# Kernel optimization log

Hardware: AMD Instinct MI355X
Metric: run time of the kernel (lower is better)

Reference implementation:

```python
import jax, jax.numpy as jnp
import numpy as np

B, S, F_IN = 8, 2048, 1024
H, SC = 512, 256
N_LAYERS = 3


def _glorot(key, shape):
    fan_in, fan_out = shape[-2], shape[-1]
    lim = float(np.sqrt(6.0 / (fan_in + fan_out)))
    return jax.random.uniform(key, shape, jnp.float32, -lim, lim)


def setup_inputs() -> dict:
    key = jax.random.key(0)
    ks = jax.random.split(key, 8)
    x = jax.random.normal(ks[0], (B, S, F_IN), jnp.float32)
    Wp = _glorot(ks[1], (F_IN, H)); bp = jnp.zeros((H,), jnp.float32)
    gcn_W = _glorot(ks[2], (N_LAYERS, H, H)); gcn_b = jnp.zeros((N_LAYERS, H), jnp.float32)
    s1_W = _glorot(ks[3], (H, SC)); s1_b = jnp.zeros((SC,), jnp.float32)
    s2_W = _glorot(ks[4], (SC, SC // 2)); s2_b = jnp.zeros((SC // 2,), jnp.float32)
    s3_W = _glorot(ks[5], (SC // 2, 1)); s3_b = jnp.zeros((1,), jnp.float32)
    return {"x": x, "Wp": Wp, "bp": bp, "gcn_W": gcn_W, "gcn_b": gcn_b,
            "s1_W": s1_W, "s1_b": s1_b, "s2_W": s2_W, "s2_b": s2_b,
            "s3_W": s3_W, "s3_b": s3_b}


def _build_adj(seq_len):
    # tridiagonal band: self + immediate temporal neighbors
    a = jnp.eye(seq_len, dtype=jnp.float32)
    a = a + jnp.eye(seq_len, k=1, dtype=jnp.float32) + jnp.eye(seq_len, k=-1, dtype=jnp.float32)
    deg = a.sum(axis=1)
    dinv = jnp.power(deg + 1e-8, -0.5)
    # D^{-1/2} A D^{-1/2}
    return dinv[:, None] * a * dinv[None, :]


def reference(x, Wp, bp, gcn_W, gcn_b, s1_W, s1_b, s2_W, s2_b, s3_W, s3_b):
    seq_len = x.shape[1]
    adj = _build_adj(seq_len)  # [S, S]
    h = jnp.einsum('bsf,fh->bsh', x, Wp) + bp  # feature projection
    for i in range(N_LAYERS):
        support = jnp.einsum('bsh,hk->bsk', h, gcn_W[i])
        h = jnp.einsum('st,btk->bsk', adj, support) + gcn_b[i]
        if i < N_LAYERS - 1:
            h = jax.nn.relu(h)  # dropout is identity in eval mode
    z = jax.nn.relu(jnp.einsum('bsh,hc->bsc', h, s1_W) + s1_b)
    z = jax.nn.relu(jnp.einsum('bsc,cd->bsd', z, s2_W) + s2_b)
    scores = jax.nn.sigmoid(jnp.einsum('bsd,do->bso', z, s3_W) + s3_b)
    return scores[..., 0]  # [B, S]
```

## Files before the change

kernel.cpp:

```cpp
#include <hip/hip_runtime.h>
#include <hip/hip_fp16.h>
#include <cstdint>
#include <cstddef>


typedef _Float16 f16;
typedef _Float16 f16x8 __attribute__((ext_vector_type(8)));
typedef float    f32x4 __attribute__((ext_vector_type(4)));

__device__ __forceinline__ void async_cp16(const void* g, void* l) {
  __builtin_amdgcn_global_load_lds((const __attribute__((address_space(1))) void*)g,
                                   (__attribute__((address_space(3))) void*)l, 16, 0, 0);
}

__device__ __forceinline__ f16x8 splat8(f16 v) {
  f16x8 r;
#pragma unroll
  for (int e = 0; e < 8; ++e) r[e] = v;
  return r;
}

template<int BM, int BN, int WAVES_M, int WAVES_N, bool RELU, bool HAS_BIAS, int AMODE>
__global__ __launch_bounds__(256, 4) void gemm_f16_kernel(
    const void* __restrict__ Aptr, const f16* __restrict__ BT,
    f16* __restrict__ C, const float* __restrict__ bias,
    int M, int N, int K)
{
  constexpr int BK = 64;
  constexpr int WM = BM / WAVES_M;
  constexpr int WN = BN / WAVES_N;
  constexpr int TM = WM / 16;
  constexpr int TN = WN / 16;
  constexpr int ITER_A = (BM * BK) / (256 * 8);
  constexpr int ITER_B = (BN * BK) / (256 * 8);
  constexpr int S = 2048;

  __shared__ __align__(16) f16 sA[BM * BK];
  __shared__ __align__(16) f16 sB[BN * BK];

  const int tid  = threadIdx.x;
  const int lane = tid & 63;
  const int wave = tid >> 6;
  const int wm   = wave / WAVES_N;
  const int wn   = wave % WAVES_N;
  const int m0   = blockIdx.x * BM;
  const int n0   = blockIdx.y * BN;

  uint32_t offA[ITER_A][3];
  f16      cfA[ITER_A][3];
  const float dM = 0.57735026919f;
  const float dE = 0.70710678118f;
#pragma unroll
  for (int j = 0; j < ITER_A; ++j) {
    const int linear = j * 256 + tid;
    const int row = linear >> 3;
    const int q   = (linear & 7) ^ (row & 7);
    const int gm  = m0 + row;
    if constexpr (AMODE == 1) {
      offA[j][0] = (uint32_t)(((size_t)gm * K + q * 8) * 4);
    } else {
      const int s = gm & (S - 1);
      const float dsv = (s == 0 || s == S - 1) ? dE : dM;
      const float cpf = (s > 0)     ? dsv * ((s - 1 == 0) ? dE : dM)     : 0.0f;
      const float csf = dsv * dsv;
      const float cnf = (s < S - 1) ? dsv * ((s + 1 == S - 1) ? dE : dM) : 0.0f;
      const int rm1 = (s > 0)     ? gm - 1 : gm;
      const int rp1 = (s < S - 1) ? gm + 1 : gm;
      offA[j][0] = (uint32_t)(((size_t)rm1 * K + q * 8) * 2);
      offA[j][1] = (uint32_t)(((size_t)gm  * K + q * 8) * 2);
      offA[j][2] = (uint32_t)(((size_t)rp1 * K + q * 8) * 2);
      cfA[j][0] = (f16)cpf; cfA[j][1] = (f16)csf; cfA[j][2] = (f16)cnf;
    }
  }

  f32x4 acc[TM][TN];
#pragma unroll
  for (int i = 0; i < TM; ++i)
#pragma unroll
    for (int j = 0; j < TN; ++j)
      acc[i][j] = (f32x4){0.f, 0.f, 0.f, 0.f};

  const int quad = lane >> 4;
  const int l16  = lane & 15;

  for (int kt = 0; kt < K; kt += BK) {
    __syncthreads();
#pragma unroll
    for (int j = 0; j < ITER_B; ++j) {
      const int linear = j * 256 + tid;
      const int row = linear >> 3;
      const int q   = (linear & 7) ^ (row & 7);
      async_cp16(BT + (size_t)(n0 + row) * K + kt + q * 8, &sB[linear * 8]);
    }
    if constexpr (AMODE == 1) {
      const char* base = (const char*)Aptr + (size_t)kt * 4;
#pragma unroll
      for (int j = 0; j < ITER_A; ++j) {
        const float4* p = (const float4*)(base + offA[j][0]);
        const float4 a = p[0], b = p[1];
        f16x8 o;
        o[0] = (f16)a.x;  o[1] = (f16)a.y;  o[2] = (f16)a.z;  o[3] = (f16)a.w;
        o[4] = (f16)b.x;  o[5] = (f16)b.y;  o[6] = (f16)b.z;  o[7] = (f16)b.w;
        *(f16x8*)&sA[(size_t)(j * 256 + tid) * 8] = o;
      }
    } else {
      const char* base = (const char*)Aptr + (size_t)kt * 2;
#pragma unroll
      for (int j = 0; j < ITER_A; ++j) {
        f16x8 pv = *(const f16x8*)(base + offA[j][0]);
        f16x8 sv = *(const f16x8*)(base + offA[j][1]);
        f16x8 nv = *(const f16x8*)(base + offA[j][2]);
        f16x8 r = pv * splat8(cfA[j][0]);
        r += sv * splat8(cfA[j][1]);
        r += nv * splat8(cfA[j][2]);
        *(f16x8*)&sA[(size_t)(j * 256 + tid) * 8] = r;
      }
    }
    __syncthreads();

#pragma unroll
    for (int kk = 0; kk < 2; ++kk) {
      const int c = quad + kk * 4;
      f16x8 af[TM], bf[TN];
#pragma unroll
      for (int mi = 0; mi < TM; ++mi) {
        const int ml = wm * WM + mi * 16 + l16;
        af[mi] = *(const f16x8*)&sA[ml * 64 + ((c ^ (ml & 7)) * 8)];
      }
#pragma unroll
      for (int ni = 0; ni < TN; ++ni) {
        const int nl = wn * WN + ni * 16 + l16;
        bf[ni] = *(const f16x8*)&sB[nl * 64 + ((c ^ (nl & 7)) * 8)];
      }
#pragma unroll
      for (int mi = 0; mi < TM; ++mi)
#pragma unroll
        for (int ni = 0; ni < TN; ++ni)
          acc[mi][ni] = __builtin_amdgcn_mfma_f32_16x16x32_f16(
              af[mi], bf[ni], acc[mi][ni], 0, 0, 0);
    }
  }

#pragma unroll
  for (int ni = 0; ni < TN; ++ni) {
    const int nc = n0 + wn * WN + ni * 16 + l16;
    const float bv = HAS_BIAS ? bias[nc] : 0.0f;
#pragma unroll
    for (int mi = 0; mi < TM; ++mi) {
#pragma unroll
      for (int r = 0; r < 4; ++r) {
        const int mr = m0 + wm * WM + mi * 16 + quad * 4 + r;
        float v = acc[mi][ni][r] + bv;
        if (RELU) v = fmaxf(v, 0.0f);
        C[(size_t)mr * N + nc] = (f16)v;
      }
    }
  }
}

__global__ __launch_bounds__(256) void head_fused_kernel(
    const f16* __restrict__ h, const f16* __restrict__ S1T,
    const f16* __restrict__ S2T,
    const float* __restrict__ s1b, const float* __restrict__ s2b,
    const float* __restrict__ s3w, const float* __restrict__ s3b,
    float* __restrict__ out)
{
  __shared__ __align__(16) char smem[36864 + 32 * 264 * 2];
  f16* sA  = (f16*)smem;
  f16* sB  = (f16*)(smem + 4096);
  f16* zs  = (f16*)(smem + 36864);
  f16* z2s = (f16*)smem;
  f16* sB2 = (f16*)(smem + 8704);

  const int tid  = threadIdx.x;
  const int lane = tid & 63;
  const int wave = tid >> 6;
  const int quad = lane >> 4;
  const int l16  = lane & 15;
  const int m0   = blockIdx.x * 32;

  f32x4 acc[2][4];
#pragma unroll
  for (int i = 0; i < 2; ++i)
#pragma unroll
    for (int j = 0; j < 4; ++j) acc[i][j] = (f32x4){0.f, 0.f, 0.f, 0.f};

  for (int kt = 0; kt < 512; kt += 64) {
    __syncthreads();
    {
      const int linear = tid;
      const int row = linear >> 3;
      const int q   = (linear & 7) ^ (row & 7);
      async_cp16(h + (size_t)(m0 + row) * 512 + kt + q * 8, &sA[linear * 8]);
    }
#pragma unroll
    for (int j = 0; j < 8; ++j) {
      const int linear = j * 256 + tid;
      const int row = linear >> 3;
      const int q   = (linear & 7) ^ (row & 7);
      async_cp16(S1T + (size_t)row * 512 + kt + q * 8, &sB[linear * 8]);
    }
    __syncthreads();
#pragma unroll
    for (int kk = 0; kk < 2; ++kk) {
      const int c = quad + kk * 4;
      f16x8 af[2], bf[4];
#pragma unroll
      for (int mi = 0; mi < 2; ++mi) {
        const int ml = mi * 16 + l16;
        af[mi] = *(const f16x8*)&sA[ml * 64 + ((c ^ (ml & 7)) * 8)];
      }
#pragma unroll
      for (int ni = 0; ni < 4; ++ni) {
        const int nl = wave * 64 + ni * 16 + l16;
        bf[ni] = *(const f16x8*)&sB[nl * 64 + ((c ^ (nl & 7)) * 8)];
      }
#pragma unroll
      for (int mi = 0; mi < 2; ++mi)
#pragma unroll
        for (int ni = 0; ni < 4; ++ni)
          acc[mi][ni] = __builtin_amdgcn_mfma_f32_16x16x32_f16(
              af[mi], bf[ni], acc[mi][ni], 0, 0, 0);
    }
  }
#pragma unroll
  for (int ni = 0; ni < 4; ++ni) {
    const int nc = wave * 64 + ni * 16 + l16;
    const float bv = s1b[nc];
#pragma unroll
    for (int mi = 0; mi < 2; ++mi)
#pragma unroll
      for (int r = 0; r < 4; ++r) {
        const int row = mi * 16 + quad * 4 + r;
        zs[row * 264 + nc] = (f16)fmaxf(acc[mi][ni][r] + bv, 0.0f);
      }
  }
  __syncthreads();

  f32x4 acc2[2][2];
#pragma unroll
  for (int i = 0; i < 2; ++i)
#pragma unroll
    for (int j = 0; j < 2; ++j) acc2[i][j] = (f32x4){0.f, 0.f, 0.f, 0.f};

  for (int kt2 = 0; kt2 < 4; ++kt2) {
    __syncthreads();
#pragma unroll
    for (int j = 0; j < 4; ++j) {
      const int linear = j * 256 + tid;
      const int row = linear >> 3;
      const int q   = (linear & 7) ^ (row & 7);
      async_cp16(S2T + (size_t)row * 256 + kt2 * 64 + q * 8, &sB2[linear * 8]);
    }
    __syncthreads();
#pragma unroll
    for (int kk = 0; kk < 2; ++kk) {
      const int c = quad + kk * 4;
      f16x8 af[2], bf[2];
#pragma unroll
      for (int mi = 0; mi < 2; ++mi) {
        const int row = mi * 16 + l16;
        af[mi] = *(const f16x8*)&zs[row * 264 + (kt2 * 8 + c) * 8];
      }
#pragma unroll
      for (int ni = 0; ni < 2; ++ni) {
        const int nl = wave * 32 + ni * 16 + l16;
        bf[ni] = *(const f16x8*)&sB2[nl * 64 + ((c ^ (nl & 7)) * 8)];
      }
#pragma unroll
      for (int mi = 0; mi < 2; ++mi)
#pragma unroll
        for (int ni = 0; ni < 2; ++ni)
          acc2[mi][ni] = __builtin_amdgcn_mfma_f32_16x16x32_f16(
              af[mi], bf[ni], acc2[mi][ni], 0, 0, 0);
    }
  }
  __syncthreads();
#pragma unroll
  for (int ni = 0; ni < 2; ++ni) {
    const int nc = wave * 32 + ni * 16 + l16;
    const float bv = s2b[nc];
#pragma unroll
    for (int mi = 0; mi < 2; ++mi)
#pragma unroll
      for (int r = 0; r < 4; ++r) {
        const int row = mi * 16 + quad * 4 + r;
        z2s[row * 136 + nc] = (f16)fmaxf(acc2[mi][ni][r] + bv, 0.0f);
      }
  }
  __syncthreads();

  const int m  = tid >> 3;
  const int qd = tid & 7;
  float p = 0.f;
#pragma unroll
  for (int j = 0; j < 2; ++j) {
    f16x8 v = *(const f16x8*)&z2s[m * 136 + qd * 16 + j * 8];
#pragma unroll
    for (int e = 0; e < 8; ++e) p += (float)v[e] * s3w[qd * 16 + j * 8 + e];
  }
  p += __shfl_xor(p, 1);
  p += __shfl_xor(p, 2);
  p += __shfl_xor(p, 4);
  if (qd == 0) out[m0 + m] = 1.0f / (1.0f + expf(-(p + s3b[0])));
}

__global__ __launch_bounds__(256) void prep_kernel(
    const float* __restrict__ Wp, f16* __restrict__ WpT,
    const float* __restrict__ gW, f16* __restrict__ GT,
    const float* __restrict__ s1W, f16* __restrict__ S1T,
    const float* __restrict__ s2W, f16* __restrict__ S2T)
{
  __shared__ f16 s[64 * 68];
  const int tid = threadIdx.x;
  int b = blockIdx.x;

  const float* W; f16* WT; int K, N, tile;
  if (b < 128)      { W = Wp;  WT = WpT; K = 1024; N = 512; tile = b; }
  else if (b < 320) { const int i = (b - 128) >> 6;
                      W = gW + (size_t)i * 262144; WT = GT + (size_t)i * 262144;
                      K = 512; N = 512; tile = (b - 128) & 63; }
  else if (b < 352) { W = s1W; WT = S1T; K = 512; N = 256; tile = b - 320; }
  else              { W = s2W; WT = S2T; K = 256; N = 128; tile = b - 352; }

  const int nt = tile % (N >> 6);
  const int kt = tile / (N >> 6);
#pragma unroll
  for (int it = 0; it < 16; ++it) {
    const int i  = it * 256 + tid;
    const int rk = i >> 6, rn = i & 63;
    s[rn * 68 + rk] = (f16)W[(size_t)(kt * 64 + rk) * N + nt * 64 + rn];
  }
  __syncthreads();
#pragma unroll
  for (int it = 0; it < 16; ++it) {
    const int i  = it * 256 + tid;
    const int rn = i >> 6, rk = i & 63;
    WT[(size_t)(nt * 64 + rn) * K + kt * 64 + rk] = s[rn * 68 + rk];
  }
}

extern "C" void kernel_launch(void* const* d_in, const int* in_sizes, int n_in,
                              void* d_out, int out_size, void* d_ws, size_t ws_size,
                              hipStream_t stream) {
  (void)in_sizes; (void)n_in; (void)out_size; (void)ws_size;
  const float* x   = (const float*)d_in[0];
  const float* Wp  = (const float*)d_in[1];
  const float* bp  = (const float*)d_in[2];
  const float* gW  = (const float*)d_in[3];
  const float* gb  = (const float*)d_in[4];
  const float* s1W = (const float*)d_in[5];
  const float* s1b = (const float*)d_in[6];
  const float* s2W = (const float*)d_in[7];
  const float* s2b = (const float*)d_in[8];
  const float* s3W = (const float*)d_in[9];
  const float* s3b = (const float*)d_in[10];
  float* out = (float*)d_out;

  constexpr int M = 16384;
  char* ws = (char*)d_ws;
  f16* hA  = (f16*)(ws + 0);
  f16* hB  = (f16*)(ws + 16777216);
  f16* WpT = (f16*)(ws + 33554432);
  f16* GT  = (f16*)(ws + 34603008);
  f16* S1T = (f16*)(ws + 36175872);
  f16* S2T = (f16*)(ws + 36438016);

  prep_kernel<<<360, 256, 0, stream>>>(Wp, WpT, gW, GT, s1W, S1T, s2W, S2T);

  gemm_f16_kernel<32, 256, 1, 4, false, true, 1>
      <<<dim3(M / 32, 2), 256, 0, stream>>>(x, WpT, hA, bp, M, 512, 1024);

  gemm_f16_kernel<32, 256, 1, 4, true, true, 2>
      <<<dim3(M / 32, 2), 256, 0, stream>>>(hA, GT, hB, gb, M, 512, 512);
  gemm_f16_kernel<32, 256, 1, 4, true, true, 2>
      <<<dim3(M / 32, 2), 256, 0, stream>>>(hB, GT + 262144, hA, gb + 512, M, 512, 512);
  gemm_f16_kernel<32, 256, 1, 4, false, true, 2>
      <<<dim3(M / 32, 2), 256, 0, stream>>>(hA, GT + 524288, hB, gb + 1024, M, 512, 512);

  head_fused_kernel<<<M / 32, 256, 0, stream>>>(hB, S1T, S2T, s1b, s2b, s3W, s3b, out);
}
```

Before: 222.0 us.

## Enlarge GEMM tiles, load halo rows into LDS, register-prefetch fp32 input

Moves the GEMMs to 64x256 tiles with 512 threads in a 2x4 wave grid. For the GCN layers, the raw A rows plus a one-row halo are copied into LDS asynchronously, and the tridiagonal stencil is applied when fragments are read from LDS. Before, each thread did three global loads per chunk. For the projection GEMM, the next K-tile of fp32 x is prefetched into registers during the MFMA loop. The cost is more LDS reads and stencil math per fragment, repeated across the N-waves, plus higher register pressure with 512-thread blocks.

```diff
diff --git a/kernel.cpp b/kernel.cpp
--- a/kernel.cpp
+++ b/kernel.cpp
@@ -20,22 +20,24 @@
   return r;
 }
 
-template<int BM, int BN, int WAVES_M, int WAVES_N, bool RELU, bool HAS_BIAS, int AMODE>
-__global__ __launch_bounds__(256, 4) void gemm_f16_kernel(
+template<int BM, int BN, bool RELU, bool HAS_BIAS, int AMODE>
+__global__ __launch_bounds__(512, 4) void gemm_f16_kernel(
     const void* __restrict__ Aptr, const f16* __restrict__ BT,
     f16* __restrict__ C, const float* __restrict__ bias,
     int M, int N, int K)
 {
   constexpr int BK = 64;
+  constexpr int NT = 512;
+  constexpr int WAVES_M = 2, WAVES_N = 4;
   constexpr int WM = BM / WAVES_M;
   constexpr int WN = BN / WAVES_N;
   constexpr int TM = WM / 16;
   constexpr int TN = WN / 16;
-  constexpr int ITER_A = (BM * BK) / (256 * 8);
-  constexpr int ITER_B = (BN * BK) / (256 * 8);
+  constexpr int ITER_B = (BN * BK) / (NT * 8);
   constexpr int S = 2048;
-
-  __shared__ __align__(16) f16 sA[BM * BK];
+  constexpr int AROWS = (AMODE == 2) ? (BM + 2) : BM;
+
+  __shared__ __align__(16) f16 sA[AROWS * BK];
   __shared__ __align__(16) f16 sB[BN * BK];
 
   const int tid  = threadIdx.x;
@@ -45,32 +47,31 @@
   const int wn   = wave % WAVES_N;
   const int m0   = blockIdx.x * BM;
   const int n0   = blockIdx.y * BN;
-
-  uint32_t offA[ITER_A][3];
-  f16      cfA[ITER_A][3];
+  const int quad = lane >> 4;
+  const int l16  = lane & 15;
+
   const float dM = 0.57735026919f;
   const float dE = 0.70710678118f;
-#pragma unroll
-  for (int j = 0; j < ITER_A; ++j) {
-    const int linear = j * 256 + tid;
-    const int row = linear >> 3;
-    const int q   = (linear & 7) ^ (row & 7);
-    const int gm  = m0 + row;
-    if constexpr (AMODE == 1) {
-      offA[j][0] = (uint32_t)(((size_t)gm * K + q * 8) * 4);
-    } else {
-      const int s = gm & (S - 1);
+
+  f16 cf[TM][3];
+  if constexpr (AMODE == 2) {
+#pragma unroll
+    for (int mi = 0; mi < TM; ++mi) {
+      const int grow = m0 + wm * WM + mi * 16 + l16;
+      const int s = grow & (S - 1);
       const float dsv = (s == 0 || s == S - 1) ? dE : dM;
-      const float cpf = (s > 0)     ? dsv * ((s - 1 == 0) ? dE : dM)     : 0.0f;
-      const float csf = dsv * dsv;
-      const float cnf = (s < S - 1) ? dsv * ((s + 1 == S - 1) ? dE : dM) : 0.0f;
-      const int rm1 = (s > 0)     ? gm - 1 : gm;
-      const int rp1 = (s < S - 1) ? gm + 1 : gm;
-      offA[j][0] = (uint32_t)(((size_t)rm1 * K + q * 8) * 2);
-      offA[j][1] = (uint32_t)(((size_t)gm  * K + q * 8) * 2);
-      offA[j][2] = (uint32_t)(((size_t)rp1 * K + q * 8) * 2);
-      cfA[j][0] = (f16)cpf; cfA[j][1] = (f16)csf; cfA[j][2] = (f16)cnf;
-    }
+      cf[mi][0] = (f16)((s > 0)     ? dsv * ((s - 1 == 0) ? dE : dM)     : 0.0f);
+      cf[mi][1] = (f16)(dsv * dsv);
+      cf[mi][2] = (f16)((s < S - 1) ? dsv * ((s + 1 == S - 1) ? dE : dM) : 0.0f);
+    }
+  }
+
+  uint32_t offA = 0;
+  {
+    const int row = tid >> 3;
+    const int q   = (tid & 7) ^ (row & 7);
+    if constexpr (AMODE == 1)
+      offA = (uint32_t)(((size_t)(m0 + row) * K + q * 8) * 4);
   }
 
   f32x4 acc[TM][TN];
@@ -80,43 +81,54 @@
     for (int j = 0; j < TN; ++j)
       acc[i][j] = (f32x4){0.f, 0.f, 0.f, 0.f};
 
-  const int quad = lane >> 4;
-  const int l16  = lane & 15;
+  float4 pa0, pa1;
+  if constexpr (AMODE == 1) {
+    const char* base = (const char*)Aptr;
+    const float4* p = (const float4*)(base + offA);
+    pa0 = p[0]; pa1 = p[1];
+  }
 
   for (int kt = 0; kt < K; kt += BK) {
-    __syncthreads();
 #pragma unroll
     for (int j = 0; j < ITER_B; ++j) {
-      const int linear = j * 256 + tid;
+      const int linear = j * NT + tid;
       const int row = linear >> 3;
       const int q   = (linear & 7) ^ (row & 7);
       async_cp16(BT + (size_t)(n0 + row) * K + kt + q * 8, &sB[linear * 8]);
     }
     if constexpr (AMODE == 1) {
-      const char* base = (const char*)Aptr + (size_t)kt * 4;
-#pragma unroll
-      for (int j = 0; j < ITER_A; ++j) {
-        const float4* p = (const float4*)(base + offA[j][0]);
-        const float4 a = p[0], b = p[1];
-        f16x8 o;
-        o[0] = (f16)a.x;  o[1] = (f16)a.y;  o[2] = (f16)a.z;  o[3] = (f16)a.w;
-        o[4] = (f16)b.x;  o[5] = (f16)b.y;  o[6] = (f16)b.z;  o[7] = (f16)b.w;
-        *(f16x8*)&sA[(size_t)(j * 256 + tid) * 8] = o;
-      }
+      f16x8 o;
+      o[0] = (f16)pa0.x; o[1] = (f16)pa0.y; o[2] = (f16)pa0.z; o[3] = (f16)pa0.w;
+      o[4] = (f16)pa1.x; o[5] = (f16)pa1.y; o[6] = (f16)pa1.z; o[7] = (f16)pa1.w;
+      *(f16x8*)&sA[(size_t)tid * 8] = o;
     } else {
-      const char* base = (const char*)Aptr + (size_t)kt * 2;
-#pragma unroll
-      for (int j = 0; j < ITER_A; ++j) {
-        f16x8 pv = *(const f16x8*)(base + offA[j][0]);
-        f16x8 sv = *(const f16x8*)(base + offA[j][1]);
-        f16x8 nv = *(const f16x8*)(base + offA[j][2]);
-        f16x8 r = pv * splat8(cfA[j][0]);
-        r += sv * splat8(cfA[j][1]);
-        r += nv * splat8(cfA[j][2]);
-        *(f16x8*)&sA[(size_t)(j * 256 + tid) * 8] = r;
-      }
-    }
-    __syncthreads();
+      {
+        const int chunk = tid + 8;
+        const int row = chunk >> 3;
+        const int q   = (chunk & 7) ^ (row & 7);
+        async_cp16((const f16*)Aptr + (size_t)(m0 + row - 1) * K + kt + q * 8,
+                   &sA[chunk * 8]);
+      }
+      if (tid < 16) {
+        const int hi = tid >> 3;
+        const int ldsrow = hi ? (BM + 1) : 0;
+        const int i = tid & 7;
+        const int q = i ^ (ldsrow & 7);
+        int g = m0 - 1 + ldsrow;
+        g = g < 0 ? 0 : (g >= M ? M - 1 : g);
+        f16x8 v = *(const f16x8*)((const f16*)Aptr + (size_t)g * K + kt + q * 8);
+        *(f16x8*)&sA[(size_t)(ldsrow * 8 + i) * 8] = v;
+      }
+    }
+    __syncthreads();
+
+    if constexpr (AMODE == 1) {
+      if (kt + BK < K) {
+        const char* base = (const char*)Aptr + (size_t)(kt + BK) * 4;
+        const float4* p = (const float4*)(base + offA);
+        pa0 = p[0]; pa1 = p[1];
+      }
+    }
 
 #pragma unroll
     for (int kk = 0; kk < 2; ++kk) {
@@ -124,8 +136,19 @@
       f16x8 af[TM], bf[TN];
 #pragma unroll
       for (int mi = 0; mi < TM; ++mi) {
-        const int ml = wm * WM + mi * 16 + l16;
-        af[mi] = *(const f16x8*)&sA[ml * 64 + ((c ^ (ml & 7)) * 8)];
+        if constexpr (AMODE == 2) {
+          const int ldr = wm * WM + mi * 16 + l16 + 1;
+          f16x8 pv = *(const f16x8*)&sA[(ldr - 1) * 64 + ((c ^ ((ldr - 1) & 7)) * 8)];
+          f16x8 sv = *(const f16x8*)&sA[(ldr    ) * 64 + ((c ^ ((ldr    ) & 7)) * 8)];
+          f16x8 nv = *(const f16x8*)&sA[(ldr + 1) * 64 + ((c ^ ((ldr + 1) & 7)) * 8)];
+          f16x8 r = pv * splat8(cf[mi][0]);
+          r += sv * splat8(cf[mi][1]);
+          r += nv * splat8(cf[mi][2]);
+          af[mi] = r;
+        } else {
+          const int ml = wm * WM + mi * 16 + l16;
+          af[mi] = *(const f16x8*)&sA[ml * 64 + ((c ^ (ml & 7)) * 8)];
+        }
       }
 #pragma unroll
       for (int ni = 0; ni < TN; ++ni) {
@@ -139,6 +162,7 @@
           acc[mi][ni] = __builtin_amdgcn_mfma_f32_16x16x32_f16(
               af[mi], bf[ni], acc[mi][ni], 0, 0, 0);
     }
+    __syncthreads();
   }
 
 #pragma unroll
@@ -368,15 +392,15 @@
 
   prep_kernel<<<360, 256, 0, stream>>>(Wp, WpT, gW, GT, s1W, S1T, s2W, S2T);
 
-  gemm_f16_kernel<32, 256, 1, 4, false, true, 1>
-      <<<dim3(M / 32, 2), 256, 0, stream>>>(x, WpT, hA, bp, M, 512, 1024);
-
-  gemm_f16_kernel<32, 256, 1, 4, true, true, 2>
-      <<<dim3(M / 32, 2), 256, 0, stream>>>(hA, GT, hB, gb, M, 512, 512);
-  gemm_f16_kernel<32, 256, 1, 4, true, true, 2>
-      <<<dim3(M / 32, 2), 256, 0, stream>>>(hB, GT + 262144, hA, gb + 512, M, 512, 512);
-  gemm_f16_kernel<32, 256, 1, 4, false, true, 2>
-      <<<dim3(M / 32, 2), 256, 0, stream>>>(hA, GT + 524288, hB, gb + 1024, M, 512, 512);
+  gemm_f16_kernel<64, 256, false, true, 1>
+      <<<dim3(M / 64, 2), 512, 0, stream>>>(x, WpT, hA, bp, M, 512, 1024);
+
+  gemm_f16_kernel<64, 256, true, true, 2>
+      <<<dim3(M / 64, 2), 512, 0, stream>>>(hA, GT, hB, gb, M, 512, 512);
+  gemm_f16_kernel<64, 256, true, true, 2>
+      <<<dim3(M / 64, 2), 512, 0, stream>>>(hB, GT + 262144, hA, gb + 512, M, 512, 512);
+  gemm_f16_kernel<64, 256, false, true, 2>
+      <<<dim3(M / 64, 2), 512, 0, stream>>>(hA, GT + 524288, hB, gb + 1024, M, 512, 512);
 
   head_fused_kernel<<<M / 32, 256, 0, stream>>>(hB, S1T, S2T, s1b, s2b, s3W, s3b, out);
 }
```

New measurement: 198.2 us. 10.7% less time.
